# Optimization experiments

Measured on AMD Instinct MI355X. Metric: run time of the kernel, lower is better.

Reference implementation:

```python
import jax, jax.numpy as jnp
import numpy as np

L = 2          # num_layers
B = 64         # batch
T = 256        # seq len (== max_len)
I = 1024       # input_size
H = 1024       # hidden_size
G = 2 * H      # gate size
EPS = 1e-5


def setup_inputs() -> dict:
    key = jax.random.key(0)
    ks = jax.random.split(key, 12)
    stdv = 1.0 / np.sqrt(H)
    u = lambda k, shp: jax.random.uniform(k, shp, jnp.float32, -stdv, stdv)
    return {
        "x": jax.random.normal(ks[0], (B, T, I), jnp.float32),
        "hx": jax.random.normal(ks[1], (L, B, H), jnp.float32),
        "w_ih": u(ks[2], (L, G, I)),
        "w_hh": u(ks[3], (L, G, H)),
        "b_ih": u(ks[4], (L, G)),
        "b_hh": u(ks[5], (L, G)),
        # SeparatedBatchNorm1d affine params: weight ~ U[0,1], bias = 0 (per reset_parameters)
        "bn_i_w": jax.random.uniform(ks[6], (L, G), jnp.float32),
        "bn_i_b": jnp.zeros((L, G), jnp.float32),
        "bn_h_w": jax.random.uniform(ks[7], (L, G), jnp.float32),
        "bn_h_b": jnp.zeros((L, G), jnp.float32),
    }


def _bn(v, w, b):
    # training-mode batch norm over the batch dim (biased variance), affine
    m = jnp.mean(v, axis=0)
    var = jnp.var(v, axis=0)
    return (v - m) * jax.lax.rsqrt(var + EPS) * w + b


def reference(x, hx, w_ih, w_hh, b_ih, b_hh, bn_i_w, bn_i_b, bn_h_w, bn_h_b):
    out = x  # [B, T, I]
    for layer in range(L):
        wih, whh = w_ih[layer], w_hh[layer]
        bih, bhh = b_ih[layer], b_hh[layer]
        iw, ib = bn_i_w[layer], bn_i_b[layer]
        hw, hb = bn_h_w[layer], bn_h_b[layer]

        # precompute input projections + per-step BN outside the recurrence
        def step(h, x_t):
            in_part = _bn(x_t @ wih.T + bih, iw, ib)          # [B, 2H]
            h_part = _bn(h @ whh.T + bhh, hw, hb)             # [B, 2H]
            gates = in_part + h_part
            ug = jax.nn.sigmoid(gates[:, :H])
            og = jax.nn.relu(gates[:, H:])
            h_new = ug * h + (1.0 - ug) * og
            return h_new, h_new

        _, ys = jax.lax.scan(step, hx[layer], jnp.swapaxes(out, 0, 1))  # ys: [T, B, H]
        out = jnp.swapaxes(ys, 0, 1)  # [B, T, H]
    return out
```

## Files before the change

### kernel.cpp

```cpp
#include <hip/hip_runtime.h>
#include <hip/hip_bf16.h>
#include <hip/hip_cooperative_groups.h>

namespace cg = cooperative_groups;


typedef __attribute__((ext_vector_type(8))) short bf16x8;
typedef __attribute__((ext_vector_type(4))) float f32x4;

constexpr size_t H_USH = 64 * 1024;
constexpr size_t W_USH = 2048 * 1024;
constexpr size_t FIXED_F = (4 * H_USH + 2 * W_USH) / 2;

__device__ __forceinline__ float wave_sum(float v) {
#pragma unroll
  for (int m = 1; m < 64; m <<= 1) v += __shfl_xor(v, m, 64);
  return v;
}

__device__ __forceinline__ unsigned short f2bf(float f) {
  __hip_bfloat16 h = __float2bfloat16(f);
  return __builtin_bit_cast(unsigned short, h);
}
__device__ __forceinline__ float bf2f(unsigned short u) {
  unsigned int x = ((unsigned int)u) << 16;
  return __builtin_bit_cast(float, x);
}
__device__ __forceinline__ void split2(float v, unsigned short& hi, unsigned short& lo) {
  hi = f2bf(v);
  lo = f2bf(v - bf2f(hi));
}

__global__ __launch_bounds__(256) void wconv(
    const float* __restrict__ w, unsigned short* __restrict__ wh, unsigned short* __restrict__ wl)
{
  int i = ((blockIdx.x << 8) + threadIdx.x) << 3;
#pragma unroll
  for (int j = 0; j < 8; j += 4) {
    float4 a = *(const float4*)(w + i + j);
    ushort4 h, l;
    split2(a.x, h.x, l.x); split2(a.y, h.y, l.y);
    split2(a.z, h.z, l.z); split2(a.w, h.w, l.w);
    *(ushort4*)(wh + i + j) = h;
    *(ushort4*)(wl + i + j) = l;
  }
}

__global__ __launch_bounds__(256) void hinit(
    const float* __restrict__ hx0, unsigned short* __restrict__ hh, unsigned short* __restrict__ hl)
{
  int i = ((blockIdx.x << 8) + threadIdx.x) << 3;
#pragma unroll
  for (int j = 0; j < 8; j += 4) {
    float4 a = *(const float4*)(hx0 + i + j);
    ushort4 h, l;
    split2(a.x, h.x, l.x); split2(a.y, h.y, l.y);
    split2(a.z, h.z, l.z); split2(a.w, h.w, l.w);
    *(ushort4*)(hh + i + j) = h;
    *(ushort4*)(hl + i + j) = l;
  }
}

__global__ __launch_bounds__(256) void proj_gemm(
    const float* __restrict__ in, const float* __restrict__ w,
    float* __restrict__ P, int t0)
{
  __shared__ float As[8][132];
  __shared__ float Bs[8][132];
  const int tid = threadIdx.x;
  const int m0 = blockIdx.y << 7;
  const int n0 = blockIdx.x << 7;
  const int tm = tid >> 4, tn = tid & 15;
  const int lr = tid >> 1;
  const int lk = (tid & 1) << 2;
  const int mA = m0 + lr;
  const int bb = mA & 63;
  const int tg = t0 + (mA >> 6);
  const float* arow = in + ((size_t)bb << 18) + ((size_t)tg << 10) + lk;
  const float* brow = w + ((size_t)(n0 + lr) << 10) + lk;
  float acc[2][2][4][4] = {};
  for (int k0 = 0; k0 < 1024; k0 += 8) {
    float4 av = *(const float4*)(arow + k0);
    float4 bv = *(const float4*)(brow + k0);
    __syncthreads();
    As[lk + 0][lr] = av.x; As[lk + 1][lr] = av.y; As[lk + 2][lr] = av.z; As[lk + 3][lr] = av.w;
    Bs[lk + 0][lr] = bv.x; Bs[lk + 1][lr] = bv.y; Bs[lk + 2][lr] = bv.z; Bs[lk + 3][lr] = bv.w;
    __syncthreads();
#pragma unroll
    for (int kk = 0; kk < 8; ++kk) {
      float4 a0 = *(const float4*)&As[kk][tm << 2];
      float4 a1 = *(const float4*)&As[kk][(tm << 2) + 64];
      float4 b0 = *(const float4*)&Bs[kk][tn << 2];
      float4 b1 = *(const float4*)&Bs[kk][(tn << 2) + 64];
      const float* ap0 = (const float*)&a0;
      const float* ap1 = (const float*)&a1;
      const float* bp0 = (const float*)&b0;
      const float* bp1 = (const float*)&b1;
#pragma unroll
      for (int i = 0; i < 4; ++i)
#pragma unroll
        for (int j = 0; j < 4; ++j) {
          acc[0][0][i][j] = fmaf(ap0[i], bp0[j], acc[0][0][i][j]);
          acc[0][1][i][j] = fmaf(ap0[i], bp1[j], acc[0][1][i][j]);
          acc[1][0][i][j] = fmaf(ap1[i], bp0[j], acc[1][0][i][j]);
          acc[1][1][i][j] = fmaf(ap1[i], bp1[j], acc[1][1][i][j]);
        }
    }
  }
#pragma unroll
  for (int mi = 0; mi < 2; ++mi)
#pragma unroll
    for (int i = 0; i < 4; ++i) {
      int m = m0 + (mi << 6) + (tm << 2) + i;
      float* prow = P + ((size_t)m << 11) + n0 + (tn << 2);
      *(float4*)prow        = make_float4(acc[mi][0][i][0], acc[mi][0][i][1], acc[mi][0][i][2], acc[mi][0][i][3]);
      *(float4*)(prow + 64) = make_float4(acc[mi][1][i][0], acc[mi][1][i][1], acc[mi][1][i][2], acc[mi][1][i][3]);
    }
}

__global__ __launch_bounds__(256) void bn_stats(
    const float* __restrict__ P, const float* __restrict__ iw, const float* __restrict__ ib,
    float* __restrict__ sc, float* __restrict__ sh)
{
  const int t = blockIdx.y;
  const int g = (blockIdx.x << 8) + threadIdx.x;
  const float* col = P + (((size_t)t << 6) << 11) + g;
  float s = 0.f, q = 0.f;
#pragma unroll 8
  for (int b = 0; b < 64; ++b) { float v = col[(size_t)b << 11]; s += v; q = fmaf(v, v, q); }
  float m = s * 0.015625f;
  float var = fmaf(-m, m, q * 0.015625f);
  float scale = iw[g] * rsqrtf(var + 1e-5f);
  sc[(t << 11) + g] = scale;
  sh[(t << 11) + g] = fmaf(-m, scale, ib[g]);
}

__global__ __launch_bounds__(512, 2) void recur_mfma(
    unsigned short* __restrict__ hAh, unsigned short* __restrict__ hAl,
    unsigned short* __restrict__ hBh, unsigned short* __restrict__ hBl,
    const unsigned short* __restrict__ wbh, const unsigned short* __restrict__ wbl,
    const float* __restrict__ P, const float* __restrict__ sc, const float* __restrict__ sh,
    const float* __restrict__ hww, const float* __restrict__ hwb,
    const float* __restrict__ hx0, float* __restrict__ out, int t0, int TS)
{
  cg::grid_group grid = cg::this_grid();
  __shared__ float part[8 * 16 * 68];
  __shared__ float lout[64 * 20];
  const int tid = threadIdx.x;
  const int lane = tid & 63;
  const int w = tid >> 6;
  const int tile = w >> 2, kq = w & 3;
  const int c0 = blockIdx.x << 4;
  const int l15 = lane & 15;
  const int koct = (lane >> 4) << 3;

  const int gcol = c0 + l15 + (tile << 10);
  const int kbase = (kq << 8) + koct;
  const size_t woff = ((size_t)gcol << 10) + kbase;
  bf16x8 whr[8], wlr[8];
#pragma unroll
  for (int ks = 0; ks < 8; ++ks) {
    whr[ks] = *(const bf16x8*)(wbh + woff + (ks << 5));
    wlr[ks] = *(const bf16x8*)(wbl + woff + (ks << 5));
  }

  const int b = lane, cs = w;
  const float wwu0 = hww[c0 + cs],        wbu0 = hwb[c0 + cs];
  const float wwu1 = hww[c0 + cs + 8],    wbu1 = hwb[c0 + cs + 8];
  const float wwo0 = hww[c0 + cs + 1024], wbo0 = hwb[c0 + cs + 1024];
  const float wwo1 = hww[c0 + cs + 1032], wbo1 = hwb[c0 + cs + 1032];

  float hold0, hold1;
  if (t0 == 0) {
    hold0 = hx0[(b << 10) + c0 + cs];
    hold1 = hx0[(b << 10) + c0 + cs + 8];
  } else {
    const size_t r = (((size_t)(b << 8)) + (t0 - 1)) << 10;
    hold0 = out[r + c0 + cs];
    hold1 = out[r + c0 + cs + 8];
  }

  const size_t aoffbase = ((size_t)l15 << 10) + kbase;

  for (int tL = 0; tL < TS; ++tL) {
    const int t = t0 + tL;
    const unsigned short *hh, *hl;
    unsigned short *oh, *ol;
    if (t & 1) { hh = hBh; hl = hBl; oh = hAh; ol = hAl; }
    else       { hh = hAh; hl = hAl; oh = hBh; ol = hBl; }

    const size_t prow = ((size_t)((tL << 6) + b)) << 11;
    const float pvu0 = P[prow + c0 + cs];
    const float pvu1 = P[prow + c0 + cs + 8];
    const float pvo0 = P[prow + c0 + cs + 1024];
    const float pvo1 = P[prow + c0 + cs + 1032];
    const float scu0 = sc[(tL << 11) + c0 + cs],        shu0 = sh[(tL << 11) + c0 + cs];
    const float scu1 = sc[(tL << 11) + c0 + cs + 8],    shu1 = sh[(tL << 11) + c0 + cs + 8];
    const float sco0 = sc[(tL << 11) + c0 + cs + 1024], sho0 = sh[(tL << 11) + c0 + cs + 1024];
    const float sco1 = sc[(tL << 11) + c0 + cs + 1032], sho1 = sh[(tL << 11) + c0 + cs + 1032];

    const unsigned short* ah = hh + aoffbase;
    const unsigned short* al = hl + aoffbase;
    f32x4 ac0 = {0.f, 0.f, 0.f, 0.f}, ac1 = ac0, ac2 = ac0, ac3 = ac0;
#pragma unroll
    for (int ks = 0; ks < 8; ++ks) {
      const int ko = ks << 5;
      bf16x8 a0h = *(const bf16x8*)(ah + ko);
      bf16x8 a1h = *(const bf16x8*)(ah + ko + (16 << 10));
      bf16x8 a2h = *(const bf16x8*)(ah + ko + (32 << 10));
      bf16x8 a3h = *(const bf16x8*)(ah + ko + (48 << 10));
      bf16x8 a0l = *(const bf16x8*)(al + ko);
      bf16x8 a1l = *(const bf16x8*)(al + ko + (16 << 10));
      bf16x8 a2l = *(const bf16x8*)(al + ko + (32 << 10));
      bf16x8 a3l = *(const bf16x8*)(al + ko + (48 << 10));
      ac0 = __builtin_amdgcn_mfma_f32_16x16x32_bf16(a0h, whr[ks], ac0, 0, 0, 0);
      ac1 = __builtin_amdgcn_mfma_f32_16x16x32_bf16(a1h, whr[ks], ac1, 0, 0, 0);
      ac2 = __builtin_amdgcn_mfma_f32_16x16x32_bf16(a2h, whr[ks], ac2, 0, 0, 0);
      ac3 = __builtin_amdgcn_mfma_f32_16x16x32_bf16(a3h, whr[ks], ac3, 0, 0, 0);
      ac0 = __builtin_amdgcn_mfma_f32_16x16x32_bf16(a0l, whr[ks], ac0, 0, 0, 0);
      ac1 = __builtin_amdgcn_mfma_f32_16x16x32_bf16(a1l, whr[ks], ac1, 0, 0, 0);
      ac2 = __builtin_amdgcn_mfma_f32_16x16x32_bf16(a2l, whr[ks], ac2, 0, 0, 0);
      ac3 = __builtin_amdgcn_mfma_f32_16x16x32_bf16(a3l, whr[ks], ac3, 0, 0, 0);
      ac0 = __builtin_amdgcn_mfma_f32_16x16x32_bf16(a0h, wlr[ks], ac0, 0, 0, 0);
      ac1 = __builtin_amdgcn_mfma_f32_16x16x32_bf16(a1h, wlr[ks], ac1, 0, 0, 0);
      ac2 = __builtin_amdgcn_mfma_f32_16x16x32_bf16(a2h, wlr[ks], ac2, 0, 0, 0);
      ac3 = __builtin_amdgcn_mfma_f32_16x16x32_bf16(a3h, wlr[ks], ac3, 0, 0, 0);
    }
    {
      float* sp = part + (w * 16 + l15) * 68 + ((lane >> 4) << 2);
      *(f32x4*)(sp +  0) = ac0;
      *(f32x4*)(sp + 16) = ac1;
      *(f32x4*)(sp + 32) = ac2;
      *(f32x4*)(sp + 48) = ac3;
    }
    __syncthreads();

#pragma unroll
    for (int half = 0; half < 2; ++half) {
      const int csub = cs + (half << 3);
      float du = part[(0 * 16 + csub) * 68 + b] + part[(1 * 16 + csub) * 68 + b] +
                 part[(2 * 16 + csub) * 68 + b] + part[(3 * 16 + csub) * 68 + b];
      float dv = part[(4 * 16 + csub) * 68 + b] + part[(5 * 16 + csub) * 68 + b] +
                 part[(6 * 16 + csub) * 68 + b] + part[(7 * 16 + csub) * 68 + b];
      float su = wave_sum(du), qu = wave_sum(du * du);
      float so = wave_sum(dv), qo = wave_sum(dv * dv);
      float mu = su * 0.015625f, vu = fmaf(-mu, mu, qu * 0.015625f);
      float mo = so * 0.015625f, vo = fmaf(-mo, mo, qo * 0.015625f);
      float hpu = (du - mu) * ((half ? wwu1 : wwu0) * rsqrtf(vu + 1e-5f)) + (half ? wbu1 : wbu0);
      float hpo = (dv - mo) * ((half ? wwo1 : wwo0) * rsqrtf(vo + 1e-5f)) + (half ? wbo1 : wbo0);
      float inu = fmaf(half ? pvu1 : pvu0, half ? scu1 : scu0, half ? shu1 : shu0);
      float ino = fmaf(half ? pvo1 : pvo0, half ? sco1 : sco0, half ? sho1 : sho0);
      float ug = 1.f / (1.f + expf(-(inu + hpu)));
      float og = fmaxf(ino + hpo, 0.f);
      float hold = half ? hold1 : hold0;
      float hnew = fmaf(ug, hold - og, og);
      if (half) hold1 = hnew; else hold0 = hnew;
      lout[b * 20 + csub] = hnew;
    }
    __syncthreads();

    if (tid < 256) {
      const int b2 = tid >> 2, q = tid & 3;
      float4 v = *(const float4*)&lout[b2 * 20 + (q << 2)];
      *(float4*)(out + (((size_t)(b2 << 8) + t) << 10) + c0 + (q << 2)) = v;
      ushort4 h4, l4;
      split2(v.x, h4.x, l4.x); split2(v.y, h4.y, l4.y);
      split2(v.z, h4.z, l4.z); split2(v.w, h4.w, l4.w);
      *(ushort4*)(oh + ((size_t)b2 << 10) + c0 + (q << 2)) = h4;
      *(ushort4*)(ol + ((size_t)b2 << 10) + c0 + (q << 2)) = l4;
    }
    grid.sync();
  }
}

extern "C" void kernel_launch(void* const* d_in, const int* in_sizes, int n_in,
                              void* d_out, int out_size, void* d_ws, size_t ws_size,
                              hipStream_t stream) {
  const float* x   = (const float*)d_in[0];
  const float* hx  = (const float*)d_in[1];
  const float* wih = (const float*)d_in[2];
  const float* whh = (const float*)d_in[3];
  const float* biw = (const float*)d_in[6];
  const float* bib = (const float*)d_in[7];
  const float* bhw = (const float*)d_in[8];
  const float* bhb = (const float*)d_in[9];
  float* out = (float*)d_out;

  const size_t wsf = ws_size / 4;
  int TS = 256;
  while (TS > 2) {
    size_t need = FIXED_F + (size_t)TS * (131072 + 4096);
    if (need <= wsf) break;
    TS >>= 1;
  }
  unsigned short* hAh = (unsigned short*)d_ws;
  unsigned short* hAl = hAh + H_USH;
  unsigned short* hBh = hAl + H_USH;
  unsigned short* hBl = hBh + H_USH;
  unsigned short* wbh = hBl + H_USH;
  unsigned short* wbl = wbh + W_USH;
  float* P  = (float*)d_ws + FIXED_F;
  float* sc = P + (size_t)TS * 131072;
  float* sh = sc + (size_t)TS * 2048;

  for (int layer = 0; layer < 2; ++layer) {
    const float* inp   = layer ? (const float*)out : x;
    const float* wih_l = wih + (size_t)layer * 2048 * 1024;
    const float* whh_l = whh + (size_t)layer * 2048 * 1024;
    const float* biw_l = biw + layer * 2048;
    const float* bib_l = bib + layer * 2048;
    const float* bhw_l = bhw + layer * 2048;
    const float* bhb_l = bhb + layer * 2048;
    const float* hx_l  = hx + (size_t)layer * 65536;

    wconv<<<dim3(1024), 256, 0, stream>>>(whh_l, wbh, wbl);
    hinit<<<dim3(32), 256, 0, stream>>>(hx_l, hAh, hAl);

    for (int t0 = 0; t0 < 256; t0 += TS) {
      proj_gemm<<<dim3(16, TS / 2), 256, 0, stream>>>(inp, wih_l, P, t0);
      bn_stats<<<dim3(8, TS), 256, 0, stream>>>(P, biw_l, bib_l, sc, sh);
      int ts = TS;
      void* args[] = { (void*)&hAh, (void*)&hAl, (void*)&hBh, (void*)&hBl,
                       (void*)&wbh, (void*)&wbl, (void*)&P, (void*)&sc, (void*)&sh,
                       (void*)&bhw_l, (void*)&bhb_l, (void*)&hx_l, (void*)&out,
                       (void*)&t0, (void*)&ts };
      hipLaunchCooperativeKernel((void*)recur_mfma, dim3(64), dim3(512), args, 0, stream);
    }
  }
}
```

Measured before the change: 15.57 ms.

## Replace cooperative grid sync with per-step per-block release/acquire flags

Drops cg::grid_group and the cooperative launch. Each block now publishes a per-timestep flag with an agent-scope release store, and at the next step waits on all 64 block flags with acquire loads and s_sleep. This is meant to cut the cost of a full grid barrier per timestep and the cooperative-launch overhead. It also pins the weight registers with empty asm to stop rematerialisation. The risk is that co-residency of the 64 blocks is no longer guaranteed by a cooperative launch, so the spin-waits could deadlock if the blocks are not all scheduled at once.

Result: faster. 13.24 ms (-14.9%).

```diff
diff --git a/kernel.cpp b/kernel.cpp
--- a/kernel.cpp
+++ b/kernel.cpp
@@ -1,8 +1,5 @@
 #include <hip/hip_runtime.h>
 #include <hip/hip_bf16.h>
-#include <hip/hip_cooperative_groups.h>
-
-namespace cg = cooperative_groups;
 
 
 typedef __attribute__((ext_vector_type(8))) short bf16x8;
@@ -11,6 +8,7 @@
 constexpr size_t H_USH = 64 * 1024;
 constexpr size_t W_USH = 2048 * 1024;
 constexpr size_t FIXED_F = (4 * H_USH + 2 * W_USH) / 2;
+constexpr size_t FLAGS_U = 2 * 256 * 64;
 
 __device__ __forceinline__ float wave_sum(float v) {
 #pragma unroll
@@ -141,9 +139,9 @@
     const unsigned short* __restrict__ wbh, const unsigned short* __restrict__ wbl,
     const float* __restrict__ P, const float* __restrict__ sc, const float* __restrict__ sh,
     const float* __restrict__ hww, const float* __restrict__ hwb,
-    const float* __restrict__ hx0, float* __restrict__ out, int t0, int TS)
-{
-  cg::grid_group grid = cg::this_grid();
+    const float* __restrict__ hx0, float* __restrict__ out,
+    unsigned* flags, int layer, int t0, int TS)
+{
   __shared__ float part[8 * 16 * 68];
   __shared__ float lout[64 * 20];
   const int tid = threadIdx.x;
@@ -163,6 +161,11 @@
     whr[ks] = *(const bf16x8*)(wbh + woff + (ks << 5));
     wlr[ks] = *(const bf16x8*)(wbl + woff + (ks << 5));
   }
+#pragma unroll
+  for (int ks = 0; ks < 8; ++ks) {
+    asm volatile("" : "+v"(whr[ks]));
+    asm volatile("" : "+v"(wlr[ks]));
+  }
 
   const int b = lane, cs = w;
   const float wwu0 = hww[c0 + cs],        wbu0 = hwb[c0 + cs];
@@ -184,6 +187,16 @@
 
   for (int tL = 0; tL < TS; ++tL) {
     const int t = t0 + tL;
+
+    if (tL > 0) {
+      if (tid < 64) {
+        const unsigned* f = flags + ((((size_t)layer << 8) + (t - 1)) << 6);
+        while (__hip_atomic_load(&f[tid], __ATOMIC_ACQUIRE, __HIP_MEMORY_SCOPE_AGENT) == 0u)
+          __builtin_amdgcn_s_sleep(2);
+      }
+      __syncthreads();
+    }
+
     const unsigned short *hh, *hl;
     unsigned short *oh, *ol;
     if (t & 1) { hh = hBh; hl = hBl; oh = hAh; ol = hAl; }
@@ -269,7 +282,10 @@
       *(ushort4*)(oh + ((size_t)b2 << 10) + c0 + (q << 2)) = h4;
       *(ushort4*)(ol + ((size_t)b2 << 10) + c0 + (q << 2)) = l4;
     }
-    grid.sync();
+    __syncthreads();
+    if (tid == 0)
+      __hip_atomic_store(flags + ((((size_t)layer << 8) + t) << 6) + blockIdx.x, 1u,
+                         __ATOMIC_RELEASE, __HIP_MEMORY_SCOPE_AGENT);
   }
 }
 
@@ -289,7 +305,7 @@
   const size_t wsf = ws_size / 4;
   int TS = 256;
   while (TS > 2) {
-    size_t need = FIXED_F + (size_t)TS * (131072 + 4096);
+    size_t need = FIXED_F + (size_t)TS * (131072 + 4096) + FLAGS_U;
     if (need <= wsf) break;
     TS >>= 1;
   }
@@ -302,6 +318,9 @@
   float* P  = (float*)d_ws + FIXED_F;
   float* sc = P + (size_t)TS * 131072;
   float* sh = sc + (size_t)TS * 2048;
+  unsigned* flags = (unsigned*)(sh + (size_t)TS * 2048);
+
+  hipMemsetAsync(flags, 0, FLAGS_U * sizeof(unsigned), stream);
 
   for (int layer = 0; layer < 2; ++layer) {
     const float* inp   = layer ? (const float*)out : x;
@@ -319,12 +338,9 @@
     for (int t0 = 0; t0 < 256; t0 += TS) {
       proj_gemm<<<dim3(16, TS / 2), 256, 0, stream>>>(inp, wih_l, P, t0);
       bn_stats<<<dim3(8, TS), 256, 0, stream>>>(P, biw_l, bib_l, sc, sh);
-      int ts = TS;
-      void* args[] = { (void*)&hAh, (void*)&hAl, (void*)&hBh, (void*)&hBl,
-                       (void*)&wbh, (void*)&wbl, (void*)&P, (void*)&sc, (void*)&sh,
-                       (void*)&bhw_l, (void*)&bhb_l, (void*)&hx_l, (void*)&out,
-                       (void*)&t0, (void*)&ts };
-      hipLaunchCooperativeKernel((void*)recur_mfma, dim3(64), dim3(512), args, 0, stream);
-    }
-  }
-}
+      recur_mfma<<<dim3(64), 512, 0, stream>>>(hAh, hAl, hBh, hBl, wbh, wbl,
+                                               P, sc, sh, bhw_l, bhb_l, hx_l, out,
+                                               flags, layer, t0, TS);
+    }
+  }
+}
```
